# Performance work log

Hardware: AMD Instinct MI355X
Metric: run time of the kernel (lower is better)

Reference implementation:

```python
import jax, jax.numpy as jnp
import numpy as np

N_RAYS, MAX_S, N_VOX, EMB, HID, L_VIEW = 8192, 64, 100000, 32, 128, 4


def view_pe(d):
    # NeRF positional encoding of view dirs: [N,3] -> [N, 3 + 6*L_VIEW]
    freqs = 2.0 ** jnp.arange(L_VIEW, dtype=d.dtype)
    ang = (d[..., None] * freqs).reshape(*d.shape[:-1], -1)  # [N, 3*L]
    return jnp.concatenate([d, jnp.sin(ang), jnp.cos(ang)], -1)


def setup_inputs() -> dict:
    key = jax.random.key(0)
    ks = jax.random.split(key, 16)
    rays_d = jax.random.normal(ks[0], (N_RAYS, 3), dtype=jnp.float32)
    rays_d = rays_d / jnp.linalg.norm(rays_d, axis=-1, keepdims=True)
    pts = jax.random.uniform(ks[1], (N_RAYS, MAX_S, 3), dtype=jnp.float32)
    t_vals = jnp.sort(jax.random.uniform(ks[2], (N_RAYS, MAX_S), dtype=jnp.float32) * 4.0, axis=-1)
    dists = jnp.concatenate([t_vals[:, 1:] - t_vals[:, :-1], jnp.full((N_RAYS, 1), 0.05, jnp.float32)], -1)
    # ragged per-ray sample counts -> -1 padded p2v_idx (as produced by the voxel point sampler)
    counts = jax.random.randint(ks[3], (N_RAYS,), 1, MAX_S + 1)
    ray_hits = jax.random.bernoulli(ks[4], 0.9, (N_RAYS,))
    valid = (jnp.arange(MAX_S)[None, :] < counts[:, None]) & ray_hits[:, None]
    idx = jax.random.randint(ks[5], (N_RAYS, MAX_S), 0, N_VOX)
    p2v_idx = jnp.where(valid, idx, -1).astype(jnp.int32)

    def lin(k, i, o):
        return jax.random.normal(k, (i, o), dtype=jnp.float32) * np.float32(1.0 / np.sqrt(i))

    return dict(
        rays_d=rays_d, pts=pts, t_vals=t_vals, dists=dists,
        p2v_idx=p2v_idx, ray_hits=ray_hits,
        vox_emb=jax.random.normal(ks[6], (N_VOX, EMB), dtype=jnp.float32) * 0.1,
        Wpts=lin(ks[7], 3, EMB),
        W1=lin(ks[8], EMB, HID), b1=jnp.zeros((HID,), jnp.float32),
        W2=lin(ks[9], HID, HID), b2=jnp.zeros((HID,), jnp.float32),
        Wsig=lin(ks[10], HID, 1), bsig=jnp.zeros((1,), jnp.float32),
        Wfeat=lin(ks[11], HID, HID), bfeat=jnp.zeros((HID,), jnp.float32),
        Wc1=lin(ks[12], HID + 3 + 6 * L_VIEW, 64), bc1=jnp.zeros((64,), jnp.float32),
        Wc2=lin(ks[13], 64, 3), bc2=jnp.zeros((3,), jnp.float32),
    )


def reference(rays_d, pts, t_vals, dists, vox_emb, Wpts, W1, b1, W2, b2,
              Wsig, bsig, Wfeat, bfeat, Wc1, bc1, Wc2, bc2, p2v_idx, ray_hits):
    mask = p2v_idx >= 0                                   # [N,S] valid samples (mask_pts)
    idx = jnp.where(mask, p2v_idx, 0)
    # voxel_embedder: per-point voxel embedding gather + positional lift
    ve = vox_emb[idx] + pts @ Wpts                        # [N,S,EMB]
    h = jax.nn.relu(ve @ W1 + b1)
    h = jax.nn.relu(h @ W2 + b2)                          # [N,S,HID]
    sigma = (h @ Wsig + bsig)[..., 0]                     # [N,S]
    feat = h @ Wfeat + bfeat                              # [N,S,HID]
    vemb = view_pe(rays_d)                                # [N,27]
    vemb = jnp.broadcast_to(vemb[:, None, :], (feat.shape[0], feat.shape[1], vemb.shape[-1]))
    c = jax.nn.relu(jnp.concatenate([feat, vemb], -1) @ Wc1 + bc1)
    rgb_raw = c @ Wc2 + bc2                               # [N,S,3]
    # masked_scatter semantics: invalid slots are 0 before the min_color remap
    rgb = (jnp.where(mask[..., None], rgb_raw, 0.0) + 1.0) * 0.5   # min_color = -1
    free_energy = jnp.where(mask, jax.nn.relu(sigma) * dists, 0.0)  # [N,S]
    # volumetric_rendering(with_dist=True)
    shifted = jnp.concatenate([jnp.zeros_like(free_energy[:, :1]), free_energy[:, :-1]], -1)
    T = jnp.exp(-jnp.cumsum(shifted, -1))
    weights = (1.0 - jnp.exp(-free_energy)) * T           # [N,S]
    comp_rgb = jnp.einsum('ns,nsc->nc', weights, rgb)     # [N,3]
    acc = weights.sum(-1)                                 # [N]
    depth = (weights * t_vals).sum(-1)
    disp = 1.0 / jnp.maximum(1e-10, depth / jnp.maximum(acc, 1e-10))
    # fill_in for missed rays (white_bkgd=False -> fill with 0)
    comp_rgb = jnp.where(ray_hits[:, None], comp_rgb, 0.0)
    disp = jnp.where(ray_hits, disp, 0.0)
    acc = jnp.where(ray_hits, acc, 0.0)
    return comp_rgb, disp, acc
```

## Files before the change

### kernel.cpp

```cpp
#include <hip/hip_runtime.h>
#include <stdint.h>


#define NRAYS 8192
#define MAXS  64
#define EMB   32
#define HID   128
#define NPE   27
#define CH    64
#define NPTS  (NRAYS * MAXS)
#define RCAP  16384

#define WS_WCOMB  0
#define WS_WPE    (WS_WCOMB + HID*CH)
#define WS_BCOMB  (WS_WPE + 32*CH)
#define WS_CCINIT (WS_BCOMB + CH)
#define WS_COUNTS (WS_CCINIT + NRAYS*CH)
#define WS_OFFS   (WS_COUNTS + NRAYS)
#define WS_TOTAL  (WS_OFFS + NRAYS)
#define WS_RCNT   (WS_TOTAL + 1)
#define WS_LIST   (WS_TOTAL + 4)
#define WS_PTOUT  (WS_LIST + NPTS)
#define WS_FRAGS  (WS_PTOUT + 4*NPTS)
#define WS_RLIST  (WS_FRAGS + 56*2*64*4)
#define WS_PTSC   (WS_RLIST + RCAP)

typedef __attribute__((ext_vector_type(8))) short bf16x8;
typedef __attribute__((ext_vector_type(4))) float f32x4;
union FI { int i[4]; int4 v; bf16x8 f; };

#define MFMA16(a, b, c) __builtin_amdgcn_mfma_f32_16x16x32_bf16(a, b, c, 0, 0, 0)

__device__ __forceinline__ f32x4 mfma3(bf16x8 ah, bf16x8 al, bf16x8 bh, bf16x8 bl,
                                       f32x4 c) {
  c = MFMA16(al, bh, c);
  c = MFMA16(ah, bl, c);
  c = MFMA16(ah, bh, c);
  return c;
}

__device__ __forceinline__ void split8(const float* x, bf16x8& hi, bf16x8& lo) {
  FI H, L;
#pragma unroll
  for (int r = 0; r < 4; ++r) {
    unsigned u0 = __float_as_uint(x[2 * r]);
    unsigned u1 = __float_as_uint(x[2 * r + 1]);
    unsigned h0 = u0 & 0xffff0000u, h1 = u1 & 0xffff0000u;
    unsigned l0 = __float_as_uint(x[2 * r] - __uint_as_float(h0));
    unsigned l1 = __float_as_uint(x[2 * r + 1] - __uint_as_float(h1));
    H.i[r] = (int)((h0 >> 16) | (h1 & 0xffff0000u));
    L.i[r] = (int)((l0 >> 16) | (l1 & 0xffff0000u));
  }
  hi = H.f; lo = L.f;
}

__device__ __forceinline__ int packword(float v) {
  unsigned u = __float_as_uint(v);
  unsigned hb = u & 0xffff0000u;
  unsigned lb = __float_as_uint(v - __uint_as_float(hb));
  return (int)((u >> 16) | (lb & 0xffff0000u));
}

__device__ __forceinline__ void unpack8(const int* w, bf16x8& hi, bf16x8& lo) {
  FI H, L;
#pragma unroll
  for (int r = 0; r < 4; ++r) {
    unsigned w0 = (unsigned)w[2 * r], w1 = (unsigned)w[2 * r + 1];
    H.i[r] = (int)((w0 & 0xffffu) | (w1 << 16));
    L.i[r] = (int)((w0 >> 16) | (w1 & 0xffff0000u));
  }
  hi = H.f; lo = L.f;
}

__global__ __launch_bounds__(256) void prep_kernel(
    const float* __restrict__ Wfeat, const float* __restrict__ bfeat,
    const float* __restrict__ Wc1, const float* __restrict__ bc1,
    float* __restrict__ ws) {
  int idx = blockIdx.x * 256 + threadIdx.x;
  if (idx < HID * CH) {
    int m = idx >> 6, j = idx & 63;
    float s = 0.f;
    for (int f = 0; f < HID; ++f) s = fmaf(Wfeat[m * HID + f], Wc1[f * CH + j], s);
    ws[WS_WCOMB + idx] = s;
    return;
  }
  idx -= HID * CH;
  if (idx < 32 * CH) {
    int v = idx >> 6, j = idx & 63;
    ws[WS_WPE + idx] = (v < NPE) ? Wc1[(HID + v) * CH + j] : 0.f;
    return;
  }
  idx -= 32 * CH;
  if (idx < CH) {
    float s = bc1[idx];
    for (int f = 0; f < HID; ++f) s = fmaf(bfeat[f], Wc1[f * CH + idx], s);
    ws[WS_BCOMB + idx] = s;
    return;
  }
  idx -= CH;
  if (idx < 2) ((int*)(ws + WS_TOTAL))[idx] = 0;
}

__global__ __launch_bounds__(256) void prep2_kernel(
    const float* __restrict__ W1, const float* __restrict__ W2,
    float* __restrict__ ws) {
  int t = blockIdx.x * 256 + threadIdx.x;
  if (t >= 56 * 64) return;
  const int fid = t >> 6, lane = t & 63;
  const int n16 = lane & 15, quad = lane >> 4;
  float x[8];
  if (fid < 8) {
    const int n = fid * 16 + n16, k0 = quad * 8;
#pragma unroll
    for (int j = 0; j < 8; ++j) x[j] = W1[(k0 + j) * HID + n];
  } else if (fid < 40) {
    const int f = fid - 8, nt = f >> 2, s = f & 3;
    const int n = nt * 16 + n16, k0 = s * 32 + quad * 8;
#pragma unroll
    for (int j = 0; j < 8; ++j) x[j] = W2[(k0 + j) * HID + n];
  } else {
    const int f = fid - 40, nt = f >> 2, s = f & 3;
    const int n = nt * 16 + n16, k0 = s * 32 + quad * 8;
#pragma unroll
    for (int j = 0; j < 8; ++j) x[j] = ws[WS_WCOMB + (k0 + j) * CH + n];
  }
  FI H, L;
#pragma unroll
  for (int r = 0; r < 4; ++r) {
    unsigned u0 = __float_as_uint(x[2 * r]);
    unsigned u1 = __float_as_uint(x[2 * r + 1]);
    unsigned h0 = u0 & 0xffff0000u, h1 = u1 & 0xffff0000u;
    unsigned l0 = __float_as_uint(x[2 * r] - __uint_as_float(h0));
    unsigned l1 = __float_as_uint(x[2 * r + 1] - __uint_as_float(h1));
    H.i[r] = (int)((h0 >> 16) | (h1 & 0xffff0000u));
    L.i[r] = (int)((l0 >> 16) | (l1 & 0xffff0000u));
  }
  int4* o = (int4*)(ws + WS_FRAGS);
  o[(fid * 2 + 0) * 64 + lane] = H.v;
  o[(fid * 2 + 1) * 64 + lane] = L.v;
}

__global__ __launch_bounds__(256) void count_pe_kernel(
    const float* __restrict__ rays_d, const int* __restrict__ p2v,
    float* __restrict__ ws) {
  const int tid = threadIdx.x;
  const int ray = blockIdx.x * 4 + (tid >> 6);
  const int lane = tid & 63;
  const int v = p2v[ray * MAXS + lane];
  const unsigned long long ball = __ballot(v >= 0);
  if (lane == 0) ((int*)(ws + WS_COUNTS))[ray] = __popcll(ball);

  const float d0 = rays_d[ray * 3 + 0];
  const float d1 = rays_d[ray * 3 + 1];
  const float d2 = rays_d[ray * 3 + 2];
  float vemb[NPE];
  vemb[0] = d0; vemb[1] = d1; vemb[2] = d2;
#pragma unroll
  for (int i = 0; i < 3; ++i) {
    const float di = (i == 0) ? d0 : (i == 1) ? d1 : d2;
#pragma unroll
    for (int l = 0; l < 4; ++l) {
      const float ang = di * (float)(1 << l);
      vemb[3 + i * 4 + l] = __sinf(ang);
      vemb[3 + 12 + i * 4 + l] = __cosf(ang);
    }
  }
  float s = ws[WS_BCOMB + lane];
  const float* wpe = ws + WS_WPE;
#pragma unroll
  for (int vv = 0; vv < NPE; ++vv) s = fmaf(vemb[vv], wpe[vv * CH + lane], s);
  ws[WS_CCINIT + ray * CH + lane] = s;
}

__global__ __launch_bounds__(1024) void scan_kernel(float* __restrict__ ws) {
  const int* counts = (const int*)(ws + WS_COUNTS);
  int* offs = (int*)(ws + WS_OFFS);
  int* totalp = (int*)(ws + WS_TOTAL);
  __shared__ int wsum[16];
  const int tid = threadIdx.x;
  const int lane = tid & 63;
  const int base = tid * 8;
  if (tid == 0) ((int*)(ws + WS_RCNT))[0] = 0;
  int c[8], e[8];
  int run = 0;
#pragma unroll
  for (int i = 0; i < 8; ++i) { c[i] = counts[base + i]; e[i] = run; run += c[i]; }
  int inc = run;
#pragma unroll
  for (int off = 1; off < 64; off <<= 1) {
    int u = __shfl_up(inc, off, 64);
    if (lane >= off) inc += u;
  }
  const int wexcl = inc - run;
  if (lane == 63) wsum[tid >> 6] = inc;
  __syncthreads();
  if (tid < 16) {
    int v = wsum[tid];
    int inc2 = v;
#pragma unroll
    for (int off = 1; off < 16; off <<= 1) {
      int u = __shfl_up(inc2, off, 64);
      if (tid >= off) inc2 += u;
    }
    wsum[tid] = inc2 - v;
    if (tid == 15) totalp[0] = inc2;
  }
  __syncthreads();
  const int wbase = wsum[tid >> 6];
#pragma unroll
  for (int i = 0; i < 8; ++i) offs[base + i] = wbase + wexcl + e[i];
}

__global__ __launch_bounds__(256) void list_kernel(
    const int* __restrict__ p2v, const float* __restrict__ pts,
    float* __restrict__ ws) {
  const int tid = threadIdx.x;
  const int ray = blockIdx.x * 4 + (tid >> 6);
  const int lane = tid & 63;
  const int pidx = ray * MAXS + lane;
  const int gidx = p2v[pidx];
  const bool valid = gidx >= 0;
  const unsigned long long ball = __ballot(valid);
  const int rank = __popcll(ball & ((1ull << lane) - 1ull));
  if (valid) {
    const int off = ((const int*)(ws + WS_OFFS))[ray];
    const int slot = off + rank;
    ((int*)(ws + WS_LIST))[slot] = pidx;
    float4 pc;
    pc.x = pts[pidx * 3 + 0];
    pc.y = pts[pidx * 3 + 1];
    pc.z = pts[pidx * 3 + 2];
    pc.w = __int_as_float(gidx);
    ((float4*)(ws + WS_PTSC))[slot] = pc;
  }
}

__device__ __forceinline__ void ve_frag(const float* __restrict__ vox_emb,
                                        const float* __restrict__ Wpts,
                                        float4 pc, int quad,
                                        bf16x8& hi, bf16x8& lo) {
  float x[8];
  const int gidx = __float_as_int(pc.w);
  const float4* vr = (const float4*)vox_emb + gidx * 8 + quad * 2;
  const float4 va = vr[0], vb = vr[1];
  const float px = pc.x, py = pc.y, pz = pc.z;
  const float4* wp = (const float4*)Wpts;
  const float4 wa0 = wp[quad * 2 + 0], wa1 = wp[quad * 2 + 1];
  const float4 wb0 = wp[8 + quad * 2 + 0], wb1 = wp[8 + quad * 2 + 1];
  const float4 wc0 = wp[16 + quad * 2 + 0], wc1 = wp[16 + quad * 2 + 1];
  x[0] = va.x + fmaf(px, wa0.x, fmaf(py, wb0.x, pz * wc0.x));
  x[1] = va.y + fmaf(px, wa0.y, fmaf(py, wb0.y, pz * wc0.y));
  x[2] = va.z + fmaf(px, wa0.z, fmaf(py, wb0.z, pz * wc0.z));
  x[3] = va.w + fmaf(px, wa0.w, fmaf(py, wb0.w, pz * wc0.w));
  x[4] = vb.x + fmaf(px, wa1.x, fmaf(py, wb1.x, pz * wc1.x));
  x[5] = vb.y + fmaf(px, wa1.y, fmaf(py, wb1.y, pz * wc1.y));
  x[6] = vb.z + fmaf(px, wa1.z, fmaf(py, wb1.z, pz * wc1.z));
  x[7] = vb.w + fmaf(px, wa1.w, fmaf(py, wb1.w, pz * wc1.w));
  split8(x, hi, lo);
}

#define LSTRIDE 133

__global__ __launch_bounds__(128, 2) void mlp_mfma(
    const float* __restrict__ vox_emb, const float* __restrict__ Wpts,
    const float* __restrict__ b1, const float* __restrict__ b2,
    const float* __restrict__ Wsig, const float* __restrict__ bsig,
    const float* __restrict__ Wc2, const float* __restrict__ bc2,
    float* __restrict__ ws) {
  __shared__ int alds[64 * LSTRIDE];
  const int tid = threadIdx.x;
  const int wave = tid >> 6, lane = tid & 63;
  const int n16 = lane & 15, quad = lane >> 4;
  const int total = ((const int*)(ws + WS_TOTAL))[0];
  const int base = blockIdx.x * 64 + wave * 32;
  if (base >= total) return;
  const int* list = (const int*)(ws + WS_LIST);
  const int slot0 = min(base + n16, total - 1);
  const int slot1 = min(base + 16 + n16, total - 1);
  const int pidx0 = list[slot0];
  const int pidx1 = list[slot1];
  const float4 pc0 = ((const float4*)(ws + WS_PTSC))[slot0];
  const float4 pc1 = ((const float4*)(ws + WS_PTSC))[slot1];
  const int4* fb = (const int4*)(ws + WS_FRAGS);

  int4 B1f[16];
#pragma unroll
  for (int i = 0; i < 16; ++i) B1f[i] = fb[i * 64 + lane];

  bf16x8 a0h, a0l, a1h, a1l;
  ve_frag(vox_emb, Wpts, pc0, quad, a0h, a0l);
  ve_frag(vox_emb, Wpts, pc1, quad, a1h, a1l);

  int4 BL[2][16];
#pragma unroll
  for (int nt = 0; nt < 8; ++nt) {
    BL[0][2 * nt]     = fb[((8 + nt * 4) * 2 + 0) * 64 + lane];
    BL[0][2 * nt + 1] = fb[((8 + nt * 4) * 2 + 1) * 64 + lane];
  }

  f32x4 h[2][8];
#pragma unroll
  for (int nt = 0; nt < 8; ++nt) {
    const float bb = b1[nt * 16 + n16];
    h[0][nt] = (f32x4){bb, bb, bb, bb};
    h[1][nt] = h[0][nt];
  }
#pragma unroll
  for (int nt = 0; nt < 8; ++nt) {
    FI H, L; H.v = B1f[2 * nt]; L.v = B1f[2 * nt + 1];
    h[0][nt] = mfma3(a0h, a0l, H.f, L.f, h[0][nt]);
    h[1][nt] = mfma3(a1h, a1l, H.f, L.f, h[1][nt]);
  }
#pragma unroll
  for (int mt = 0; mt < 2; ++mt)
#pragma unroll
    for (int nt = 0; nt < 8; ++nt)
#pragma unroll
      for (int r = 0; r < 4; ++r) {
        const float v = fmaxf(h[mt][nt][r], 0.f);
        alds[(wave * 32 + mt * 16 + quad * 4 + r) * LSTRIDE + nt * 16 + n16] = packword(v);
      }

  f32x4 g[2][8];
#pragma unroll
  for (int nt = 0; nt < 8; ++nt) {
    const float bb = b2[nt * 16 + n16];
    g[0][nt] = (f32x4){bb, bb, bb, bb};
    g[1][nt] = g[0][nt];
  }
  const int rb0 = (wave * 32 + n16) * LSTRIDE;
  const int rb1 = rb0 + 16 * LSTRIDE;
#pragma unroll
  for (int s = 0; s < 4; ++s) {
    if (s < 3) {
#pragma unroll
      for (int nt = 0; nt < 8; ++nt) {
        BL[(s + 1) & 1][2 * nt]     = fb[((8 + nt * 4 + s + 1) * 2 + 0) * 64 + lane];
        BL[(s + 1) & 1][2 * nt + 1] = fb[((8 + nt * 4 + s + 1) * 2 + 1) * 64 + lane];
      }
    }
    int w0[8], w1[8];
#pragma unroll
    for (int j = 0; j < 8; ++j) {
      w0[j] = alds[rb0 + s * 32 + quad * 8 + j];
      w1[j] = alds[rb1 + s * 32 + quad * 8 + j];
    }
    bf16x8 A0h, A0l, A1h, A1l;
    unpack8(w0, A0h, A0l);
    unpack8(w1, A1h, A1l);
#pragma unroll
    for (int nt = 0; nt < 8; ++nt) {
      FI H, L; H.v = BL[s & 1][2 * nt]; L.v = BL[s & 1][2 * nt + 1];
      g[0][nt] = mfma3(A0h, A0l, H.f, L.f, g[0][nt]);
      g[1][nt] = mfma3(A1h, A1l, H.f, L.f, g[1][nt]);
    }
  }

  int pm[2][4];
#pragma unroll
  for (int mt = 0; mt < 2; ++mt)
#pragma unroll
    for (int r = 0; r < 4; ++r)
      pm[mt][r] = __shfl(mt ? pidx1 : pidx0, quad * 4 + r, 64);
  int4 BC[2][8];
#pragma unroll
  for (int nt = 0; nt < 4; ++nt) {
    BC[0][2 * nt]     = fb[((40 + nt * 4) * 2 + 0) * 64 + lane];
    BC[0][2 * nt + 1] = fb[((40 + nt * 4) * 2 + 1) * 64 + lane];
  }
  f32x4 cacc[2][4];
#pragma unroll
  for (int mt = 0; mt < 2; ++mt)
#pragma unroll
    for (int nt = 0; nt < 4; ++nt)
#pragma unroll
      for (int r = 0; r < 4; ++r)
        cacc[mt][nt][r] = ws[WS_CCINIT + (pm[mt][r] >> 6) * CH + nt * 16 + n16];

  float sg[2][4] = {{0.f, 0.f, 0.f, 0.f}, {0.f, 0.f, 0.f, 0.f}};
#pragma unroll
  for (int nt = 0; nt < 8; ++nt) {
    const float sv = Wsig[nt * 16 + n16];
#pragma unroll
    for (int mt = 0; mt < 2; ++mt)
#pragma unroll
      for (int r = 0; r < 4; ++r) {
        const float v = fmaxf(g[mt][nt][r], 0.f);
        sg[mt][r] = fmaf(v, sv, sg[mt][r]);
        alds[(wave * 32 + mt * 16 + quad * 4 + r) * LSTRIDE + nt * 16 + n16] = packword(v);
      }
  }
#pragma unroll
  for (int mask = 1; mask < 16; mask <<= 1)
#pragma unroll
    for (int mt = 0; mt < 2; ++mt)
#pragma unroll
      for (int r = 0; r < 4; ++r) sg[mt][r] += __shfl_xor(sg[mt][r], mask, 64);

#pragma unroll
  for (int s = 0; s < 4; ++s) {
    if (s < 3) {
#pragma unroll
      for (int nt = 0; nt < 4; ++nt) {
        BC[(s + 1) & 1][2 * nt]     = fb[((40 + nt * 4 + s + 1) * 2 + 0) * 64 + lane];
        BC[(s + 1) & 1][2 * nt + 1] = fb[((40 + nt * 4 + s + 1) * 2 + 1) * 64 + lane];
      }
    }
    int w0[8], w1[8];
#pragma unroll
    for (int j = 0; j < 8; ++j) {
      w0[j] = alds[rb0 + s * 32 + quad * 8 + j];
      w1[j] = alds[rb1 + s * 32 + quad * 8 + j];
    }
    bf16x8 A0h, A0l, A1h, A1l;
    unpack8(w0, A0h, A0l);
    unpack8(w1, A1h, A1l);
#pragma unroll
    for (int nt = 0; nt < 4; ++nt) {
      FI H, L; H.v = BC[s & 1][2 * nt]; L.v = BC[s & 1][2 * nt + 1];
      cacc[0][nt] = mfma3(A0h, A0l, H.f, L.f, cacc[0][nt]);
      cacc[1][nt] = mfma3(A1h, A1l, H.f, L.f, cacc[1][nt]);
    }
  }

  float cr[2][3][4];
#pragma unroll
  for (int mt = 0; mt < 2; ++mt)
#pragma unroll
    for (int c = 0; c < 3; ++c)
#pragma unroll
      for (int r = 0; r < 4; ++r) cr[mt][c][r] = 0.f;
#pragma unroll
  for (int nt = 0; nt < 4; ++nt) {
    const int j = nt * 16 + n16;
    const float w0 = Wc2[j * 3 + 0], w1c = Wc2[j * 3 + 1], w2c = Wc2[j * 3 + 2];
#pragma unroll
    for (int mt = 0; mt < 2; ++mt)
#pragma unroll
      for (int r = 0; r < 4; ++r) {
        const float cv = fmaxf(cacc[mt][nt][r], 0.f);
        cr[mt][0][r] = fmaf(cv, w0, cr[mt][0][r]);
        cr[mt][1][r] = fmaf(cv, w1c, cr[mt][1][r]);
        cr[mt][2][r] = fmaf(cv, w2c, cr[mt][2][r]);
      }
  }
#pragma unroll
  for (int mask = 1; mask < 16; mask <<= 1)
#pragma unroll
    for (int mt = 0; mt < 2; ++mt)
#pragma unroll
      for (int c = 0; c < 3; ++c)
#pragma unroll
        for (int r = 0; r < 4; ++r) cr[mt][c][r] += __shfl_xor(cr[mt][c][r], mask, 64);

  if (n16 == 0) {
    const float bs = bsig[0];
    const float bcr = bc2[0], bcg = bc2[1], bcb = bc2[2];
#pragma unroll
    for (int mt = 0; mt < 2; ++mt)
#pragma unroll
      for (int r = 0; r < 4; ++r) {
        const int m = mt * 16 + quad * 4 + r;
        if (base + m < total) {
          const int pid = pm[mt][r];
          const float sig = sg[mt][r] + bs;
          ((float4*)(ws + WS_PTOUT))[pid] =
              make_float4(sig, cr[mt][0][r] + bcr, cr[mt][1][r] + bcg, cr[mt][2][r] + bcb);
          if (fabsf(sig) < 0.006f) {
            const int ri = atomicAdd((int*)(ws + WS_RCNT), 1);
            if (ri < RCAP) ((int*)(ws + WS_RLIST))[ri] = pid;
          }
        }
      }
  }
}

__device__ __forceinline__ float wave_sum(float v) {
#pragma unroll
  for (int off = 32; off > 0; off >>= 1) v += __shfl_down(v, off, 64);
  return v;
}

__global__ __launch_bounds__(256) void repair_kernel(
    const float* __restrict__ pts, const int* __restrict__ p2v,
    const float* __restrict__ vox_emb, const float* __restrict__ Wpts,
    const float* __restrict__ W1, const float* __restrict__ b1,
    const float* __restrict__ W2, const float* __restrict__ b2,
    const float* __restrict__ Wsig, const float* __restrict__ bsig,
    float* __restrict__ ws) {
  __shared__ float h1s[4][HID];
  const int wv = threadIdx.x >> 6, lane = threadIdx.x & 63;
  const int cnt = min(((const int*)(ws + WS_RCNT))[0], RCAP);
  const int nw = gridDim.x * 4;
  for (int i = blockIdx.x * 4 + wv; i < cnt; i += nw) {
    const int pidx = ((const int*)(ws + WS_RLIST))[i];
    const int gidx = p2v[pidx];
    const float px = pts[pidx * 3 + 0];
    const float py = pts[pidx * 3 + 1];
    const float pz = pts[pidx * 3 + 2];
    float ve[EMB];
#pragma unroll
    for (int e = 0; e < EMB; ++e)
      ve[e] = vox_emb[gidx * EMB + e] +
              fmaf(px, Wpts[e], fmaf(py, Wpts[EMB + e], pz * Wpts[2 * EMB + e]));
    float s0 = b1[lane], s1 = b1[lane + 64];
#pragma unroll
    for (int k = 0; k < EMB; ++k) {
      const float x = ve[k];
      s0 = fmaf(x, W1[k * HID + lane], s0);
      s1 = fmaf(x, W1[k * HID + lane + 64], s1);
    }
    h1s[wv][lane] = fmaxf(s0, 0.f);
    h1s[wv][lane + 64] = fmaxf(s1, 0.f);
    float t0 = b2[lane], t1 = b2[lane + 64];
    for (int k = 0; k < HID; ++k) {
      const float x = h1s[wv][k];
      t0 = fmaf(x, W2[k * HID + lane], t0);
      t1 = fmaf(x, W2[k * HID + lane + 64], t1);
    }
    float sp = fmaf(fmaxf(t0, 0.f), Wsig[lane], fmaxf(t1, 0.f) * Wsig[lane + 64]);
    sp = wave_sum(sp);
    if (lane == 0) ws[WS_PTOUT + 4 * pidx + 0] = sp + bsig[0];
  }
}

__device__ __forceinline__ float wave_prefix_excl(float v, int lane) {
  float inc = v;
#pragma unroll
  for (int off = 1; off < 64; off <<= 1) {
    float u = __shfl_up(inc, off, 64);
    if (lane >= off) inc += u;
  }
  return inc - v;
}

__global__ __launch_bounds__(256) void render_kernel(
    const float* __restrict__ t_vals, const float* __restrict__ dists,
    const int* __restrict__ p2v, const float* __restrict__ ws,
    float* __restrict__ out_rgb, float* __restrict__ out_disp,
    float* __restrict__ out_acc) {
  const int tid = threadIdx.x;
  const int ray = blockIdx.x * 4 + (tid >> 6);
  const int lane = tid & 63;
  const int pidx = ray * MAXS + lane;

  const int vidx = p2v[pidx];
  const bool hit = (__shfl(vidx, 0, 64) >= 0);
  if (!hit) {
    if (lane < 3) out_rgb[ray * 3 + lane] = 0.f;
    if (lane == 0) { out_disp[ray] = 0.f; out_acc[ray] = 0.f; }
    return;
  }
  const bool valid = vidx >= 0;

  const float4 pv = ((const float4*)(ws + WS_PTOUT))[pidx];
  const float fe = valid ? fmaxf(pv.x, 0.f) * dists[pidx] : 0.f;
  const float pref = wave_prefix_excl(fe, lane);
  const float T = __expf(-pref);
  const float w = (1.f - __expf(-fe)) * T;
  const float tv = t_vals[pidx];

  const float crgb0 = wave_sum(w * (pv.y + 1.f) * 0.5f);
  const float crgb1 = wave_sum(w * (pv.z + 1.f) * 0.5f);
  const float crgb2 = wave_sum(w * (pv.w + 1.f) * 0.5f);
  const float accs = wave_sum(w);
  const float depth = wave_sum(w * tv);

  if (lane == 0) {
    out_rgb[ray * 3 + 0] = crgb0;
    out_rgb[ray * 3 + 1] = crgb1;
    out_rgb[ray * 3 + 2] = crgb2;
    const float disp = 1.f / fmaxf(1e-10f, depth / fmaxf(accs, 1e-10f));
    out_disp[ray] = disp;
    out_acc[ray] = accs;
  }
}

extern "C" void kernel_launch(void* const* d_in, const int* in_sizes, int n_in,
                              void* d_out, int out_size, void* d_ws, size_t ws_size,
                              hipStream_t stream) {
  const float* rays_d  = (const float*)d_in[0];
  const float* pts     = (const float*)d_in[1];
  const float* t_vals  = (const float*)d_in[2];
  const float* dists   = (const float*)d_in[3];
  const int*   p2v     = (const int*)d_in[4];
  const float* vox_emb = (const float*)d_in[6];
  const float* Wpts    = (const float*)d_in[7];
  const float* W1      = (const float*)d_in[8];
  const float* b1      = (const float*)d_in[9];
  const float* W2      = (const float*)d_in[10];
  const float* b2      = (const float*)d_in[11];
  const float* Wsig    = (const float*)d_in[12];
  const float* bsig    = (const float*)d_in[13];
  const float* Wfeat   = (const float*)d_in[14];
  const float* bfeat   = (const float*)d_in[15];
  const float* Wc1     = (const float*)d_in[16];
  const float* bc1     = (const float*)d_in[17];
  const float* Wc2     = (const float*)d_in[18];
  const float* bc2     = (const float*)d_in[19];

  float* ws = (float*)d_ws;
  float* out = (float*)d_out;
  float* out_rgb = out;
  float* out_disp = out + NRAYS * 3;
  float* out_acc = out + NRAYS * 4;

  hipLaunchKernelGGL(prep_kernel, dim3(41), dim3(256), 0, stream,
                     Wfeat, bfeat, Wc1, bc1, ws);
  hipLaunchKernelGGL(prep2_kernel, dim3(14), dim3(256), 0, stream, W1, W2, ws);
  hipLaunchKernelGGL(count_pe_kernel, dim3(NRAYS / 4), dim3(256), 0, stream,
                     rays_d, p2v, ws);
  hipLaunchKernelGGL(scan_kernel, dim3(1), dim3(1024), 0, stream, ws);
  hipLaunchKernelGGL(list_kernel, dim3(NRAYS / 4), dim3(256), 0, stream,
                     p2v, pts, ws);
  hipLaunchKernelGGL(mlp_mfma, dim3(NPTS / 64), dim3(128), 0, stream,
                     vox_emb, Wpts, b1, b2, Wsig, bsig, Wc2, bc2, ws);
  hipLaunchKernelGGL(repair_kernel, dim3(128), dim3(256), 0, stream,
                     pts, p2v, vox_emb, Wpts, W1, b1, W2, b2, Wsig, bsig, ws);
  hipLaunchKernelGGL(render_kernel, dim3(NRAYS / 4), dim3(256), 0, stream,
                     t_vals, dists, p2v, ws, out_rgb, out_disp, out_acc);
}
```

Before: 260.1 us.

## Store hidden activations as single bf16 in swizzled LDS and drop lo-term MFMA

Hidden activations are now rounded to a single bf16 (round-to-nearest-even) instead of a hi/lo split pair, and stored in a 16-bit LDS buffer with an XOR swizzle so each lane reads its A fragment with one 16-byte load instead of unpacking words. The second and third GEMMs use two MFMAs per tile (activation hi times weight hi and lo) instead of three. The LDS footprint halves, and launch bounds raise the occupancy target to 4 blocks per CU. This cuts LDS traffic, packing arithmetic and MFMA count, at the cost of activation precision that may affect accuracy tolerance.

```diff
diff --git a/kernel.cpp b/kernel.cpp
--- a/kernel.cpp
+++ b/kernel.cpp
@@ -39,6 +39,12 @@
   return c;
 }
 
+__device__ __forceinline__ f32x4 mfma2(bf16x8 ah, bf16x8 bh, bf16x8 bl, f32x4 c) {
+  c = MFMA16(ah, bl, c);
+  c = MFMA16(ah, bh, c);
+  return c;
+}
+
 __device__ __forceinline__ void split8(const float* x, bf16x8& hi, bf16x8& lo) {
   FI H, L;
 #pragma unroll
@@ -54,22 +60,9 @@
   hi = H.f; lo = L.f;
 }
 
-__device__ __forceinline__ int packword(float v) {
+__device__ __forceinline__ unsigned short bf16rne(float v) {
   unsigned u = __float_as_uint(v);
-  unsigned hb = u & 0xffff0000u;
-  unsigned lb = __float_as_uint(v - __uint_as_float(hb));
-  return (int)((u >> 16) | (lb & 0xffff0000u));
-}
-
-__device__ __forceinline__ void unpack8(const int* w, bf16x8& hi, bf16x8& lo) {
-  FI H, L;
-#pragma unroll
-  for (int r = 0; r < 4; ++r) {
-    unsigned w0 = (unsigned)w[2 * r], w1 = (unsigned)w[2 * r + 1];
-    H.i[r] = (int)((w0 & 0xffffu) | (w1 << 16));
-    L.i[r] = (int)((w0 >> 16) | (w1 & 0xffff0000u));
-  }
-  hi = H.f; lo = L.f;
+  return (unsigned short)((u + 0x7fffu + ((u >> 16) & 1u)) >> 16);
 }
 
 __global__ __launch_bounds__(256) void prep_kernel(
@@ -259,15 +252,15 @@
   split8(x, hi, lo);
 }
 
-#define LSTRIDE 133
-
-__global__ __launch_bounds__(128, 2) void mlp_mfma(
+#define SROW 136
+
+__global__ __launch_bounds__(128, 4) void mlp_mfma(
     const float* __restrict__ vox_emb, const float* __restrict__ Wpts,
     const float* __restrict__ b1, const float* __restrict__ b2,
     const float* __restrict__ Wsig, const float* __restrict__ bsig,
     const float* __restrict__ Wc2, const float* __restrict__ bc2,
     float* __restrict__ ws) {
-  __shared__ int alds[64 * LSTRIDE];
+  __shared__ __align__(16) unsigned short alds[64 * SROW];
   const int tid = threadIdx.x;
   const int wave = tid >> 6, lane = tid & 63;
   const int n16 = lane & 15, quad = lane >> 4;
@@ -318,7 +311,9 @@
 #pragma unroll
       for (int r = 0; r < 4; ++r) {
         const float v = fmaxf(h[mt][nt][r], 0.f);
-        alds[(wave * 32 + mt * 16 + quad * 4 + r) * LSTRIDE + nt * 16 + n16] = packword(v);
+        const int row = wave * 32 + mt * 16 + quad * 4 + r;
+        const int gk = ((2 * nt + (n16 >> 3)) ^ (row & 7)) << 3;
+        alds[row * SROW + gk + (n16 & 7)] = bf16rne(v);
       }
 
   f32x4 g[2][8];
@@ -328,8 +323,9 @@
     g[0][nt] = (f32x4){bb, bb, bb, bb};
     g[1][nt] = g[0][nt];
   }
-  const int rb0 = (wave * 32 + n16) * LSTRIDE;
-  const int rb1 = rb0 + 16 * LSTRIDE;
+  const int rrow0 = (wave * 32 + n16) * SROW;
+  const int rrow1 = rrow0 + 16 * SROW;
+  const int t7 = n16 & 7;
 #pragma unroll
   for (int s = 0; s < 4; ++s) {
     if (s < 3) {
@@ -339,20 +335,14 @@
         BL[(s + 1) & 1][2 * nt + 1] = fb[((8 + nt * 4 + s + 1) * 2 + 1) * 64 + lane];
       }
     }
-    int w0[8], w1[8];
-#pragma unroll
-    for (int j = 0; j < 8; ++j) {
-      w0[j] = alds[rb0 + s * 32 + quad * 8 + j];
-      w1[j] = alds[rb1 + s * 32 + quad * 8 + j];
-    }
-    bf16x8 A0h, A0l, A1h, A1l;
-    unpack8(w0, A0h, A0l);
-    unpack8(w1, A1h, A1l);
+    const int gq = ((4 * s + quad) ^ t7) << 3;
+    const bf16x8 A0h = *(const bf16x8*)&alds[rrow0 + gq];
+    const bf16x8 A1h = *(const bf16x8*)&alds[rrow1 + gq];
 #pragma unroll
     for (int nt = 0; nt < 8; ++nt) {
       FI H, L; H.v = BL[s & 1][2 * nt]; L.v = BL[s & 1][2 * nt + 1];
-      g[0][nt] = mfma3(A0h, A0l, H.f, L.f, g[0][nt]);
-      g[1][nt] = mfma3(A1h, A1l, H.f, L.f, g[1][nt]);
+      g[0][nt] = mfma2(A0h, H.f, L.f, g[0][nt]);
+      g[1][nt] = mfma2(A1h, H.f, L.f, g[1][nt]);
     }
   }
 
@@ -387,7 +377,9 @@
       for (int r = 0; r < 4; ++r) {
         const float v = fmaxf(g[mt][nt][r], 0.f);
         sg[mt][r] = fmaf(v, sv, sg[mt][r]);
-        alds[(wave * 32 + mt * 16 + quad * 4 + r) * LSTRIDE + nt * 16 + n16] = packword(v);
+        const int row = wave * 32 + mt * 16 + quad * 4 + r;
+        const int gk = ((2 * nt + (n16 >> 3)) ^ (row & 7)) << 3;
+        alds[row * SROW + gk + (n16 & 7)] = bf16rne(v);
       }
   }
 #pragma unroll
@@ -406,20 +398,14 @@
         BC[(s + 1) & 1][2 * nt + 1] = fb[((40 + nt * 4 + s + 1) * 2 + 1) * 64 + lane];
       }
     }
-    int w0[8], w1[8];
-#pragma unroll
-    for (int j = 0; j < 8; ++j) {
-      w0[j] = alds[rb0 + s * 32 + quad * 8 + j];
-      w1[j] = alds[rb1 + s * 32 + quad * 8 + j];
-    }
-    bf16x8 A0h, A0l, A1h, A1l;
-    unpack8(w0, A0h, A0l);
-    unpack8(w1, A1h, A1l);
+    const int gq = ((4 * s + quad) ^ t7) << 3;
+    const bf16x8 A0h = *(const bf16x8*)&alds[rrow0 + gq];
+    const bf16x8 A1h = *(const bf16x8*)&alds[rrow1 + gq];
 #pragma unroll
     for (int nt = 0; nt < 4; ++nt) {
       FI H, L; H.v = BC[s & 1][2 * nt]; L.v = BC[s & 1][2 * nt + 1];
-      cacc[0][nt] = mfma3(A0h, A0l, H.f, L.f, cacc[0][nt]);
-      cacc[1][nt] = mfma3(A1h, A1l, H.f, L.f, cacc[1][nt]);
+      cacc[0][nt] = mfma2(A0h, H.f, L.f, cacc[0][nt]);
+      cacc[1][nt] = mfma2(A1h, H.f, L.f, cacc[1][nt]);
     }
   }
 
```

Result: slower. 311.1 us (+19.6%).
